# Optimization experiments

Hardware: AMD Instinct MI355X
Metric: run time of the kernel (lower is better)

Reference implementation:

```python
import jax, jax.numpy as jnp
import numpy as np
from jax import lax

SIGMA = 1.0
ALPHA = 1.0
BETA = 1.0
TRUNCATE = 4.0  # scipy.ndimage default


def _gauss_kernel(sigma):
    radius = int(TRUNCATE * sigma + 0.5)  # scipy radius rule -> 4 for sigma=1
    x = np.arange(-radius, radius + 1, dtype=np.float64)
    k = np.exp(-0.5 * (x / sigma) ** 2)
    k = (k / k.sum()).astype(np.float32)
    return k

_KERNEL = _gauss_kernel(SIGMA)


def _blur_axis(img, k, axis):
    # scipy mode='reflect' == jnp.pad mode='symmetric' (edge repeated)
    r = len(k) // 2
    pad = [(0, 0)] * img.ndim
    pad[axis] = (r, r)
    xp = jnp.pad(img, pad, mode='symmetric')
    n = img.shape[axis]
    out = k[0] * lax.slice_in_dim(xp, 0, n, axis=axis)
    for i in range(1, len(k)):
        out = out + k[i] * lax.slice_in_dim(xp, i, i + n, axis=axis)
    return out


def gaussian_blur(img):
    # scalar sigma in scipy blurs along EVERY axis, including batch & channel
    k = jnp.asarray(_KERNEL, dtype=img.dtype)
    for ax in range(img.ndim):
        img = _blur_axis(img, k, ax)
    return img


def decompose(I):
    I_log = jnp.log(I + 1e-6)
    I_smooth = gaussian_blur(I_log)
    R = I_log - I_smooth
    L = I_log - R  # == I_smooth
    return jnp.exp(L), jnp.exp(R)


def setup_inputs() -> dict:
    key = jax.random.key(0)
    k1, k2 = jax.random.split(key)
    shape = (16, 3, 512, 512)
    I_enhanced = jax.random.uniform(k1, shape, dtype=jnp.float32)
    I_gt = jax.random.uniform(k2, shape, dtype=jnp.float32)
    return {"I_enhanced": I_enhanced, "I_gt": I_gt}


def reference(I_enhanced, I_gt):
    L_enh, R_enh = decompose(I_enhanced)
    L_gt, R_gt = decompose(I_gt)
    L_reflectance = jnp.mean((R_enh - R_gt) ** 2)
    L_illumination = jnp.mean((L_enh - L_gt) ** 2)
    return ALPHA * L_reflectance + BETA * L_illumination
```

## Files before the change

kernel.cpp:

```cpp
#include <hip/hip_runtime.h>
#include <cmath>

#define PLANE (512*512)
#define NPLANES 48
#define NEL (48*PLANE)

struct Taps { float k[9]; };
struct CMat { float w[3][3]; };


__global__ __launch_bounds__(64)
void k_blur_hw(const float* __restrict__ inE, const float* __restrict__ inG,
               float* __restrict__ ws, Taps tp)
{
    const int l  = threadIdx.x;
    const int r0 = blockIdx.x * 32;
    const int z  = blockIdx.y;

    const float* src = (z < NPLANES) ? (inE + z * PLANE)
                                     : (inG + (z - NPLANES) * PLANE);

    const bool is0  = (l == 0);
    const bool is63 = (l == 63);
    const int  vout = (l >> 3) * 6144 + (l & 7) * 8;

    float ring[10][8];

    int rp0 = r0 - 4;
    rp0 = (rp0 < 0) ? (-1 - rp0) : ((rp0 > 511) ? (1023 - rp0) : rp0);
    float4 a = *(const float4*)(src + rp0 * 512 + l * 8);
    float4 b = *(const float4*)(src + rp0 * 512 + l * 8 + 4);

    for (int jb = 0; jb < 40; jb += 10) {
#pragma unroll
        for (int u = 0; u < 10; ++u) {
            const int j = jb + u;

            int rn = r0 - 4 + j + 1;
            rn = (rn < 0) ? (-1 - rn) : ((rn > 511) ? (1023 - rn) : rn);
            const float* nrp = src + rn * 512 + l * 8;
            float4 na = *(const float4*)nrp;
            float4 nb = *(const float4*)(nrp + 4);

            float win[16];
            win[4]  = __logf(a.x + 1e-6f);
            win[5]  = __logf(a.y + 1e-6f);
            win[6]  = __logf(a.z + 1e-6f);
            win[7]  = __logf(a.w + 1e-6f);
            win[8]  = __logf(b.x + 1e-6f);
            win[9]  = __logf(b.y + 1e-6f);
            win[10] = __logf(b.z + 1e-6f);
            win[11] = __logf(b.w + 1e-6f);

            float s;
            s = __shfl_up(win[8], 1);   win[0]  = is0  ? win[7]  : s;
            s = __shfl_up(win[9], 1);   win[1]  = is0  ? win[6]  : s;
            s = __shfl_up(win[10], 1);  win[2]  = is0  ? win[5]  : s;
            s = __shfl_up(win[11], 1);  win[3]  = is0  ? win[4]  : s;
            s = __shfl_down(win[4], 1); win[12] = is63 ? win[11] : s;
            s = __shfl_down(win[5], 1); win[13] = is63 ? win[10] : s;
            s = __shfl_down(win[6], 1); win[14] = is63 ? win[9]  : s;
            s = __shfl_down(win[7], 1); win[15] = is63 ? win[8]  : s;

#pragma unroll
            for (int i = 0; i < 8; ++i) {
                float o = 0.f;
#pragma unroll
                for (int t = 0; t < 9; ++t) o += tp.k[t] * win[i + t];
                ring[u][i] = o;
            }

            if (j >= 8) {
                float acc[8];
#pragma unroll
                for (int i = 0; i < 8; ++i) {
                    float o = 0.f;
#pragma unroll
                    for (int t = 0; t < 9; ++t)
                        o += tp.k[t] * ring[(u + 2 + t) % 10][i];
                    acc[i] = o;
                }
                const int ro = r0 + j - 8;
                float* dp = ws + (ro * 768 + z) * 64 + vout;
                *(float4*)dp       = make_float4(acc[0], acc[1], acc[2], acc[3]);
                *(float4*)(dp + 4) = make_float4(acc[4], acc[5], acc[6], acc[7]);
            }
            a = na; b = nb;
        }
    }
}

__global__ __launch_bounds__(256)
void k_cn_loss(const float* __restrict__ ws, const float* __restrict__ Ie,
               const float* __restrict__ Ig, float* __restrict__ part,
               Taps tp, CMat cm)
{
    const int tid = threadIdx.x;
    const int hw  = blockIdx.x * 256 + tid;
    const float* wbase = ws + (hw >> 6) * (96 * 64) + (hw & 63);

    float re[9][3];
    float rg[9][3];

#define LOADCB(m, ring, OFF)                                                   \
    {                                                                          \
        float v0 = wbase[((OFF) + (m) * 3 + 0) * 64];                          \
        float v1 = wbase[((OFF) + (m) * 3 + 1) * 64];                          \
        float v2 = wbase[((OFF) + (m) * 3 + 2) * 64];                          \
        ring[(m) % 9][0] = cm.w[0][0]*v0 + cm.w[0][1]*v1 + cm.w[0][2]*v2;      \
        ring[(m) % 9][1] = cm.w[1][0]*v0 + cm.w[1][1]*v1 + cm.w[1][2]*v2;      \
        ring[(m) % 9][2] = cm.w[2][0]*v0 + cm.w[2][1]*v1 + cm.w[2][2]*v2;      \
    }

#pragma unroll
    for (int m = 0; m < 4; ++m) { LOADCB(m, re, 0); LOADCB(m, rg, 48); }

    float acc = 0.f;
#pragma unroll
    for (int n = 0; n < 16; ++n) {
        const int mnew = n + 4;
        if (mnew < 16) { LOADCB(mnew, re, 0); LOADCB(mnew, rg, 48); }
#pragma unroll
        for (int c = 0; c < 3; ++c) {
            float se = 0.f, sg = 0.f;
#pragma unroll
            for (int t = 0; t < 9; ++t) {
                int m = n - 4 + t;
                m = (m < 0) ? (-1 - m) : ((m > 15) ? (31 - m) : m);
                se += tp.k[t] * re[m % 9][c];
                sg += tp.k[t] * rg[m % 9][c];
            }
            const int j = n * 3 + c;
            float ie = Ie[j * PLANE + hw] + 1e-6f;
            float ig = Ig[j * PLANE + hw] + 1e-6f;
            float ee = __expf(-se);
            float eg = __expf(-sg);
            float Re = ie * ee;
            float Rg = ig * eg;
            float Le = __builtin_amdgcn_rcpf(ee);
            float Lg = __builtin_amdgcn_rcpf(eg);
            float dr = Re - Rg;
            float dl = Le - Lg;
            acc += dr * dr + dl * dl;
        }
    }
#undef LOADCB

    __shared__ float red[256];
    red[tid] = acc;
    __syncthreads();
#pragma unroll
    for (int s = 128; s > 0; s >>= 1) {
        if (tid < s) red[tid] += red[tid + s];
        __syncthreads();
    }
    if (tid == 0) part[blockIdx.x] = red[0];
}

__global__ __launch_bounds__(256)
void k_final(const float* __restrict__ part, float* __restrict__ out)
{
    __shared__ float red[256];
    float a = 0.f;
    for (int i = threadIdx.x; i < 1024; i += 256) a += part[i];
    red[threadIdx.x] = a;
    __syncthreads();
#pragma unroll
    for (int s = 128; s > 0; s >>= 1) {
        if (threadIdx.x < s) red[threadIdx.x] += red[threadIdx.x + s];
        __syncthreads();
    }
    if (threadIdx.x == 0) out[0] = red[0] * (1.0f / (float)NEL);
}

extern "C" void kernel_launch(void* const* d_in, const int* in_sizes, int n_in,
                              void* d_out, int out_size, void* d_ws, size_t ws_size,
                              hipStream_t stream) {
    const float* Ie = (const float*)d_in[0];
    const float* Ig = (const float*)d_in[1];

    Taps tp;
    {
        double kk[9], s = 0.0;
        for (int i = 0; i < 9; ++i) { double x = (double)(i - 4); kk[i] = exp(-0.5 * x * x); s += kk[i]; }
        for (int i = 0; i < 9; ++i) tp.k[i] = (float)(kk[i] / s);
    }

    CMat cm;
    {
        for (int c = 0; c < 3; ++c) {
            cm.w[c][0] = cm.w[c][1] = cm.w[c][2] = 0.f;
            for (int t = 0; t < 9; ++t) {
                int m = c - 4 + t;
                int mm = ((m % 6) + 6) % 6;
                if (mm > 2) mm = 5 - mm;
                cm.w[c][mm] += tp.k[t];
            }
        }
    }

    float* ws   = (float*)d_ws;
    float* part = ws + 2 * (size_t)NEL;

    dim3 g1(16, 96);
    k_blur_hw<<<g1, 64, 0, stream>>>(Ie, Ig, ws, tp);
    k_cn_loss<<<1024, 256, 0, stream>>>(ws, Ie, Ig, part, tp, cm);
    k_final<<<1, 256, 0, stream>>>(part, (float*)d_out);
}
```

Before: 181.7 us.

## Shrink blur row tiles for more blocks and software-prefetch loads in loss kernel

The HW blur kernel now processes 8 output rows per block instead of 32, giving 4x more blocks (64x96 grid), fully unrolling a 16-row loop with a 9-entry ring, and adding a min-blocks launch bound. This raises parallelism and occupancy for a grid that previously had only 1536 single-wave blocks, at the cost of more redundant halo rows (16 rows read per 8 output rows). The loss kernel now prefetches the next workspace channel group and the next Ie/Ig inputs one iteration ahead, hiding global load latency behind the exp/blur arithmetic at the cost of extra registers.

```diff
diff --git a/kernel.cpp b/kernel.cpp
--- a/kernel.cpp
+++ b/kernel.cpp
@@ -9,12 +9,12 @@
 struct CMat { float w[3][3]; };
 
 
-__global__ __launch_bounds__(64)
+__global__ __launch_bounds__(64, 4)
 void k_blur_hw(const float* __restrict__ inE, const float* __restrict__ inG,
                float* __restrict__ ws, Taps tp)
 {
     const int l  = threadIdx.x;
-    const int r0 = blockIdx.x * 32;
+    const int r0 = blockIdx.x * 8;
     const int z  = blockIdx.y;
 
     const float* src = (z < NPLANES) ? (inE + z * PLANE)
@@ -24,69 +24,65 @@
     const bool is63 = (l == 63);
     const int  vout = (l >> 3) * 6144 + (l & 7) * 8;
 
-    float ring[10][8];
+    float ring[9][8];
 
     int rp0 = r0 - 4;
-    rp0 = (rp0 < 0) ? (-1 - rp0) : ((rp0 > 511) ? (1023 - rp0) : rp0);
+    rp0 = (rp0 < 0) ? (-1 - rp0) : rp0;
     float4 a = *(const float4*)(src + rp0 * 512 + l * 8);
     float4 b = *(const float4*)(src + rp0 * 512 + l * 8 + 4);
 
-    for (int jb = 0; jb < 40; jb += 10) {
-#pragma unroll
-        for (int u = 0; u < 10; ++u) {
-            const int j = jb + u;
-
-            int rn = r0 - 4 + j + 1;
-            rn = (rn < 0) ? (-1 - rn) : ((rn > 511) ? (1023 - rn) : rn);
-            const float* nrp = src + rn * 512 + l * 8;
-            float4 na = *(const float4*)nrp;
-            float4 nb = *(const float4*)(nrp + 4);
-
-            float win[16];
-            win[4]  = __logf(a.x + 1e-6f);
-            win[5]  = __logf(a.y + 1e-6f);
-            win[6]  = __logf(a.z + 1e-6f);
-            win[7]  = __logf(a.w + 1e-6f);
-            win[8]  = __logf(b.x + 1e-6f);
-            win[9]  = __logf(b.y + 1e-6f);
-            win[10] = __logf(b.z + 1e-6f);
-            win[11] = __logf(b.w + 1e-6f);
-
-            float s;
-            s = __shfl_up(win[8], 1);   win[0]  = is0  ? win[7]  : s;
-            s = __shfl_up(win[9], 1);   win[1]  = is0  ? win[6]  : s;
-            s = __shfl_up(win[10], 1);  win[2]  = is0  ? win[5]  : s;
-            s = __shfl_up(win[11], 1);  win[3]  = is0  ? win[4]  : s;
-            s = __shfl_down(win[4], 1); win[12] = is63 ? win[11] : s;
-            s = __shfl_down(win[5], 1); win[13] = is63 ? win[10] : s;
-            s = __shfl_down(win[6], 1); win[14] = is63 ? win[9]  : s;
-            s = __shfl_down(win[7], 1); win[15] = is63 ? win[8]  : s;
-
+#pragma unroll
+    for (int j = 0; j < 16; ++j) {
+        int rn = r0 - 4 + j + 1;
+        rn = (rn < 0) ? (-1 - rn) : ((rn > 511) ? (1023 - rn) : rn);
+        const float* nrp = src + rn * 512 + l * 8;
+        float4 na = *(const float4*)nrp;
+        float4 nb = *(const float4*)(nrp + 4);
+
+        float win[16];
+        win[4]  = __logf(a.x + 1e-6f);
+        win[5]  = __logf(a.y + 1e-6f);
+        win[6]  = __logf(a.z + 1e-6f);
+        win[7]  = __logf(a.w + 1e-6f);
+        win[8]  = __logf(b.x + 1e-6f);
+        win[9]  = __logf(b.y + 1e-6f);
+        win[10] = __logf(b.z + 1e-6f);
+        win[11] = __logf(b.w + 1e-6f);
+
+        float s;
+        s = __shfl_up(win[8], 1);   win[0]  = is0  ? win[7]  : s;
+        s = __shfl_up(win[9], 1);   win[1]  = is0  ? win[6]  : s;
+        s = __shfl_up(win[10], 1);  win[2]  = is0  ? win[5]  : s;
+        s = __shfl_up(win[11], 1);  win[3]  = is0  ? win[4]  : s;
+        s = __shfl_down(win[4], 1); win[12] = is63 ? win[11] : s;
+        s = __shfl_down(win[5], 1); win[13] = is63 ? win[10] : s;
+        s = __shfl_down(win[6], 1); win[14] = is63 ? win[9]  : s;
+        s = __shfl_down(win[7], 1); win[15] = is63 ? win[8]  : s;
+
+#pragma unroll
+        for (int i = 0; i < 8; ++i) {
+            float o = 0.f;
+#pragma unroll
+            for (int t = 0; t < 9; ++t) o += tp.k[t] * win[i + t];
+            ring[j % 9][i] = o;
+        }
+
+        if (j >= 8) {
+            float acc[8];
 #pragma unroll
             for (int i = 0; i < 8; ++i) {
                 float o = 0.f;
 #pragma unroll
-                for (int t = 0; t < 9; ++t) o += tp.k[t] * win[i + t];
-                ring[u][i] = o;
-            }
-
-            if (j >= 8) {
-                float acc[8];
-#pragma unroll
-                for (int i = 0; i < 8; ++i) {
-                    float o = 0.f;
-#pragma unroll
-                    for (int t = 0; t < 9; ++t)
-                        o += tp.k[t] * ring[(u + 2 + t) % 10][i];
-                    acc[i] = o;
-                }
-                const int ro = r0 + j - 8;
-                float* dp = ws + (ro * 768 + z) * 64 + vout;
-                *(float4*)dp       = make_float4(acc[0], acc[1], acc[2], acc[3]);
-                *(float4*)(dp + 4) = make_float4(acc[4], acc[5], acc[6], acc[7]);
-            }
-            a = na; b = nb;
-        }
+                for (int t = 0; t < 9; ++t)
+                    o += tp.k[t] * ring[(j - 8 + t) % 9][i];
+                acc[i] = o;
+            }
+            const int ro = r0 + j - 8;
+            float* dp = ws + (ro * 768 + z) * 64 + vout;
+            *(float4*)dp       = make_float4(acc[0], acc[1], acc[2], acc[3]);
+            *(float4*)(dp + 4) = make_float4(acc[4], acc[5], acc[6], acc[7]);
+        }
+        a = na; b = nb;
     }
 }
 
@@ -102,24 +98,50 @@
     float re[9][3];
     float rg[9][3];
 
-#define LOADCB(m, ring, OFF)                                                   \
-    {                                                                          \
-        float v0 = wbase[((OFF) + (m) * 3 + 0) * 64];                          \
-        float v1 = wbase[((OFF) + (m) * 3 + 1) * 64];                          \
-        float v2 = wbase[((OFF) + (m) * 3 + 2) * 64];                          \
-        ring[(m) % 9][0] = cm.w[0][0]*v0 + cm.w[0][1]*v1 + cm.w[0][2]*v2;      \
-        ring[(m) % 9][1] = cm.w[1][0]*v0 + cm.w[1][1]*v1 + cm.w[1][2]*v2;      \
-        ring[(m) % 9][2] = cm.w[2][0]*v0 + cm.w[2][1]*v1 + cm.w[2][2]*v2;      \
-    }
-
-#pragma unroll
-    for (int m = 0; m < 4; ++m) { LOADCB(m, re, 0); LOADCB(m, rg, 48); }
+#define LOADRAW(m, vE, vG)                                                     \
+    vE[0] = wbase[((m) * 3 + 0) * 64];                                         \
+    vE[1] = wbase[((m) * 3 + 1) * 64];                                         \
+    vE[2] = wbase[((m) * 3 + 2) * 64];                                         \
+    vG[0] = wbase[(48 + (m) * 3 + 0) * 64];                                    \
+    vG[1] = wbase[(48 + (m) * 3 + 1) * 64];                                    \
+    vG[2] = wbase[(48 + (m) * 3 + 2) * 64];
+
+#define CBLUR(v, dst)                                                          \
+    dst[0] = cm.w[0][0] * v[0] + cm.w[0][1] * v[1] + cm.w[0][2] * v[2];        \
+    dst[1] = cm.w[1][0] * v[0] + cm.w[1][1] * v[1] + cm.w[1][2] * v[2];        \
+    dst[2] = cm.w[2][0] * v[0] + cm.w[2][1] * v[1] + cm.w[2][2] * v[2];
+
+#pragma unroll
+    for (int m = 0; m < 4; ++m) {
+        float vE[3], vG[3];
+        LOADRAW(m, vE, vG);
+        CBLUR(vE, re[m]); CBLUR(vG, rg[m]);
+    }
+    float nvE[3], nvG[3];
+    LOADRAW(4, nvE, nvG);
+    float ieq[3], igq[3];
+#pragma unroll
+    for (int c = 0; c < 3; ++c) {
+        ieq[c] = Ie[c * PLANE + hw] + 1e-6f;
+        igq[c] = Ig[c * PLANE + hw] + 1e-6f;
+    }
 
     float acc = 0.f;
 #pragma unroll
     for (int n = 0; n < 16; ++n) {
+        float nie[3], nig[3];
+        if (n + 1 < 16) {
+#pragma unroll
+            for (int c = 0; c < 3; ++c) {
+                nie[c] = Ie[((n + 1) * 3 + c) * PLANE + hw] + 1e-6f;
+                nig[c] = Ig[((n + 1) * 3 + c) * PLANE + hw] + 1e-6f;
+            }
+        }
         const int mnew = n + 4;
-        if (mnew < 16) { LOADCB(mnew, re, 0); LOADCB(mnew, rg, 48); }
+        if (mnew < 16) {
+            CBLUR(nvE, re[mnew % 9]); CBLUR(nvG, rg[mnew % 9]);
+            if (mnew + 1 < 16) { LOADRAW(mnew + 1, nvE, nvG); }
+        }
 #pragma unroll
         for (int c = 0; c < 3; ++c) {
             float se = 0.f, sg = 0.f;
@@ -130,21 +152,23 @@
                 se += tp.k[t] * re[m % 9][c];
                 sg += tp.k[t] * rg[m % 9][c];
             }
-            const int j = n * 3 + c;
-            float ie = Ie[j * PLANE + hw] + 1e-6f;
-            float ig = Ig[j * PLANE + hw] + 1e-6f;
             float ee = __expf(-se);
             float eg = __expf(-sg);
-            float Re = ie * ee;
-            float Rg = ig * eg;
+            float Re = ieq[c] * ee;
+            float Rg = igq[c] * eg;
             float Le = __builtin_amdgcn_rcpf(ee);
             float Lg = __builtin_amdgcn_rcpf(eg);
             float dr = Re - Rg;
             float dl = Le - Lg;
             acc += dr * dr + dl * dl;
         }
-    }
-#undef LOADCB
+        if (n + 1 < 16) {
+#pragma unroll
+            for (int c = 0; c < 3; ++c) { ieq[c] = nie[c]; igq[c] = nig[c]; }
+        }
+    }
+#undef LOADRAW
+#undef CBLUR
 
     __shared__ float red[256];
     red[tid] = acc;
@@ -202,7 +226,7 @@
     float* ws   = (float*)d_ws;
     float* part = ws + 2 * (size_t)NEL;
 
-    dim3 g1(16, 96);
+    dim3 g1(64, 96);
     k_blur_hw<<<g1, 64, 0, stream>>>(Ie, Ig, ws, tp);
     k_cn_loss<<<1024, 256, 0, stream>>>(ws, Ie, Ig, part, tp, cm);
     k_final<<<1, 256, 0, stream>>>(part, (float*)d_out);
```

Result: slower. 204.7 us (+12.7%).
